# Optimization experiments

Measured on AMD Instinct MI355X. Metric: run time of the kernel, lower is better.

The kernel has to match this reference:

```python
import jax, jax.numpy as jnp
import numpy as np

G, KP, EPS = 4, 9, 1e-5  # deformable groups, 3x3 kernel points, BN eps


def setup_inputs() -> dict:
    key = jax.random.key(0)
    ks = jax.random.split(key, 16)
    N, C1, C2, H, W = 8, 256, 256, 64, 64
    c = int(C1 * 1.0) // 16 * 16  # 256 internal width
    OM = int(np.ceil(G * KP * 3 / 8) * 8)  # 112 padded offset/mask dim (108 used)
    sd = 0.02
    return {
        "x": jax.random.normal(ks[0], (N, C1, H, W), jnp.float32),
        "cv1_w": jax.random.normal(ks[1], (c, C1), jnp.float32) * sd,
        "cv1_b": jax.random.normal(ks[2], (c,), jnp.float32) * sd,
        "value_w": jax.random.normal(ks[3], (c, c), jnp.float32) * sd,
        "value_b": jax.random.normal(ks[4], (c,), jnp.float32) * sd,
        "dw_w": jax.random.normal(ks[5], (c,), jnp.float32) * sd + 1.0,
        "dw_b": jax.random.normal(ks[6], (c,), jnp.float32) * sd,
        "om_w": jax.random.normal(ks[7], (OM, c), jnp.float32) * sd,
        "om_b": jax.random.normal(ks[8], (OM,), jnp.float32) * sd,
        "out_w": jax.random.normal(ks[9], (c, c), jnp.float32) * sd,
        "cv2_w": jax.random.normal(ks[10], (C2, c), jnp.float32) * sd,
        "bn_gamma": jnp.ones((C2,), jnp.float32),
        "bn_beta": jnp.zeros((C2,), jnp.float32),
        "bn_mean": jax.random.normal(ks[11], (C2,), jnp.float32) * 0.1,
        "bn_var": jax.random.uniform(ks[12], (C2,), jnp.float32, minval=0.5, maxval=1.5),
    }


def _dcnv4(value, offset_mask, H, W):
    """DCNv4 core: offset-based bilinear sampling + unnormalized-mask aggregation.
    value: (N,H,W,c) NHWC features; offset_mask: (N,H,W,OM), per group layout
    [2*KP offsets (dx,dy pairs), KP masks]; no softmax on masks (DCNv4)."""
    N, c = value.shape[0], value.shape[-1]
    GC = c // G
    om = offset_mask[..., : G * KP * 3].reshape(N, H, W, G, 3 * KP)
    offs = om[..., : 2 * KP].reshape(N, H, W, G, KP, 2)  # (dx, dy), x = width axis
    mask = om[..., 2 * KP:]                               # (N,H,W,G,KP)
    ky, kx = jnp.meshgrid(jnp.arange(-1, 2, dtype=jnp.float32),
                          jnp.arange(-1, 2, dtype=jnp.float32), indexing="ij")
    kx, ky = kx.reshape(KP), ky.reshape(KP)               # 3x3 dilation-1 grid
    base_x = jnp.arange(W, dtype=jnp.float32)[None, None, :, None, None]
    base_y = jnp.arange(H, dtype=jnp.float32)[None, :, None, None, None]
    px = base_x + kx + offs[..., 0]                       # (N,H,W,G,KP) abs pixel x
    py = base_y + ky + offs[..., 1]
    x0, y0 = jnp.floor(px), jnp.floor(py)
    fx, fy = px - x0, py - y0
    x0i, y0i = x0.astype(jnp.int32), y0.astype(jnp.int32)
    vflat = value.reshape(N, H * W, G, GC).transpose(0, 2, 1, 3)  # (N,G,L,GC)
    acc = jnp.zeros((N, G, H, W, KP, GC), value.dtype)
    for dy, dx, wgt in ((0, 0, (1 - fy) * (1 - fx)), (0, 1, (1 - fy) * fx),
                        (1, 0, fy * (1 - fx)), (1, 1, fy * fx)):
        yy, xx = y0i + dy, x0i + dx
        valid = (yy >= 0) & (yy < H) & (xx >= 0) & (xx < W)   # zero padding
        idx = jnp.clip(yy, 0, H - 1) * W + jnp.clip(xx, 0, W - 1)
        idx_g = idx.transpose(0, 3, 1, 2, 4).reshape(N, G, H * W * KP)
        smp = jnp.take_along_axis(vflat, idx_g[..., None], axis=2)
        smp = smp.reshape(N, G, H, W, KP, GC)
        acc = acc + smp * (wgt * valid).transpose(0, 3, 1, 2, 4)[..., None]
    out = (acc * mask.transpose(0, 3, 1, 2, 4)[..., None]).sum(axis=4)  # (N,G,H,W,GC)
    return out.transpose(0, 2, 3, 1, 4).reshape(N, H, W, c)


def reference(x, cv1_w, cv1_b, value_w, value_b, dw_w, dw_b, om_w, om_b,
              out_w, cv2_w, bn_gamma, bn_beta, bn_mean, bn_var):
    N, C1, H, W = x.shape
    t = jnp.einsum("nchw,dc->nhwd", x, cv1_w) + cv1_b       # cv1 1x1 conv -> NHWC
    value = t @ value_w.T + value_b                          # DCNv4 value_proj
    om = (t * dw_w + dw_b) @ om_w.T + om_b                   # depthwise 1x1 + linear
    y = _dcnv4(value, om, H, W)
    y = y @ out_w.T                                          # output_proj (no bias)
    y = jnp.einsum("nhwc,dc->nhwd", y, cv2_w)                # cv2 1x1 (no bias)
    y = (y - bn_mean) * bn_gamma * jax.lax.rsqrt(bn_var + EPS) + bn_beta  # BN (eval)
    y = y * jax.nn.sigmoid(y)                                # SiLU
    return y.transpose(0, 3, 1, 2)                           # back to NCHW
```

## Files before the change

### kernel.cpp

```cpp
#include <hip/hip_runtime.h>
#include <hip/hip_bf16.h>
#include <math.h>

#define NN    8
#define HH    64
#define WW    64
#define HW    4096
#define NHW   32768
#define DALL  384
#define EPSBN 1e-5f

typedef __attribute__((ext_vector_type(8))) short short8v;
typedef __attribute__((ext_vector_type(4))) float f32x4;
typedef __attribute__((ext_vector_type(2))) float f32x2;

__device__ __forceinline__ float b2f(unsigned short u) {
    union { unsigned int i; float f; } v; v.i = ((unsigned int)u) << 16; return v.f;
}
__device__ __forceinline__ unsigned short f2b(float f) {
    __hip_bfloat16 h = __float2bfloat16(f);
    return *reinterpret_cast<const unsigned short*>(&h);
}
__device__ __forceinline__ f32x2 bf2x(int u) {
    union { int i; float f; } a, b;
    a.i = u << 16;
    b.i = u & 0xffff0000;
    f32x2 r; r[0] = a.f; r[1] = b.f; return r;
}


__global__ __launch_bounds__(256)
void prep_kernel(const float* __restrict__ cv1_w, const float* __restrict__ cv1_b,
                 const float* __restrict__ value_w, const float* __restrict__ value_b,
                 const float* __restrict__ dw_w, const float* __restrict__ dw_b,
                 const float* __restrict__ om_w, const float* __restrict__ om_b,
                 const float* __restrict__ out_w, const float* __restrict__ cv2_w,
                 const float* __restrict__ bn_g, const float* __restrict__ bn_b,
                 const float* __restrict__ bn_m, const float* __restrict__ bn_v,
                 unsigned short* __restrict__ Wallbf, float* __restrict__ ball,
                 unsigned short* __restrict__ Woutbf, float* __restrict__ bout)
{
    int job = blockIdx.x * 256 + threadIdx.x;
    if (job < 65536) {
        int d = job >> 8, cc = job & 255;
        float s0=0.f, s1=0.f, s2=0.f, s3=0.f;
        for (int e = 0; e < 256; e += 4) {
            float4 wv = *reinterpret_cast<const float4*>(&value_w[d*256+e]);
            s0 = fmaf(wv.x, cv1_w[(e+0)*256+cc], s0);
            s1 = fmaf(wv.y, cv1_w[(e+1)*256+cc], s1);
            s2 = fmaf(wv.z, cv1_w[(e+2)*256+cc], s2);
            s3 = fmaf(wv.w, cv1_w[(e+3)*256+cc], s3);
        }
        Wallbf[job] = f2b((s0+s1)+(s2+s3));
    } else if (job < 94208) {
        int idx = job - 65536;
        int o = idx >> 8, cc = idx & 255;
        float s0=0.f, s1=0.f, s2=0.f, s3=0.f;
        for (int e = 0; e < 256; e += 4) {
            float4 wv = *reinterpret_cast<const float4*>(&om_w[o*256+e]);
            float4 dv = *reinterpret_cast<const float4*>(&dw_w[e]);
            s0 = fmaf(wv.x*dv.x, cv1_w[(e+0)*256+cc], s0);
            s1 = fmaf(wv.y*dv.y, cv1_w[(e+1)*256+cc], s1);
            s2 = fmaf(wv.z*dv.z, cv1_w[(e+2)*256+cc], s2);
            s3 = fmaf(wv.w*dv.w, cv1_w[(e+3)*256+cc], s3);
        }
        Wallbf[job] = f2b((s0+s1)+(s2+s3));
    } else if (job < 98304) {
        Wallbf[job] = 0;
    } else if (job < 163840) {
        int idx = job - 98304;
        int d = idx >> 8, cc = idx & 255;
        float s0=0.f, s1=0.f, s2=0.f, s3=0.f;
        for (int e = 0; e < 256; e += 4) {
            float4 wv = *reinterpret_cast<const float4*>(&cv2_w[d*256+e]);
            s0 = fmaf(wv.x, out_w[(e+0)*256+cc], s0);
            s1 = fmaf(wv.y, out_w[(e+1)*256+cc], s1);
            s2 = fmaf(wv.z, out_w[(e+2)*256+cc], s2);
            s3 = fmaf(wv.w, out_w[(e+3)*256+cc], s3);
        }
        float sc = bn_g[d] * rsqrtf(bn_v[d] + EPSBN);
        Woutbf[idx] = f2b(((s0+s1)+(s2+s3)) * sc);
    } else if (job < 164096) {
        int d = job - 163840;
        float s = value_b[d];
        for (int e = 0; e < 256; ++e) s = fmaf(value_w[d*256+e], cv1_b[e], s);
        ball[d] = s;
    } else if (job < 164208) {
        int o = job - 164096;
        float s = om_b[o];
        for (int e = 0; e < 256; ++e)
            s = fmaf(om_w[o*256+e], fmaf(dw_w[e], cv1_b[e], dw_b[e]), s);
        ball[256 + o] = s;
    } else if (job < 164224) {
        ball[368 + job - 164208] = 0.f;
    } else if (job < 164480) {
        int d = job - 164224;
        float sc = bn_g[d] * rsqrtf(bn_v[d] + EPSBN);
        bout[d] = fmaf(-bn_m[d], sc, bn_b[d]);
    }
}

__global__ __launch_bounds__(256)
void gemm_vo_kernel(const float* __restrict__ x, const unsigned short* __restrict__ Wallbf,
                    const float* __restrict__ ball, unsigned short* __restrict__ VO)
{
    __shared__ unsigned short As[8192];
    __shared__ unsigned short Bs[8192];
    int t = threadIdx.x;
    int m0 = blockIdx.y * 128;
    int n0 = blockIdx.x * 128;
    int nimg = m0 >> 12, hw0 = m0 & 4095;
    int lane = t & 63;
    int wv = t >> 6;
    int wr = wv >> 1, wc = wv & 1;
    int r_l = lane & 15, kg_l = lane >> 4;
    int ci = t >> 6;
    int l  = t & 63;

    const float* xbase = x + (size_t)(nimg * 256) * 4096 + hw0;

    f32x4 acc[4][4] = {};

    for (int kt = 0; kt < 4; ++kt) {
        int c0 = kt * 64;
        float2 val[16];
        #pragma unroll
        for (int i = 0; i < 16; ++i)
            val[i] = *reinterpret_cast<const float2*>(
                &xbase[(size_t)(c0 + ci*16 + i) * 4096 + 2*l]);
        __syncthreads();
        #pragma unroll
        for (int rsel = 0; rsel < 2; ++rsel) {
            int row = 2*l + rsel;
            #pragma unroll
            for (int kgi = 0; kgi < 2; ++kgi) {
                int kg = ci*2 + kgi;
                short8v s;
                #pragma unroll
                for (int j = 0; j < 8; ++j)
                    s[j] = (short)f2b(rsel ? val[kgi*8+j].y : val[kgi*8+j].x);
                *reinterpret_cast<short8v*>(&As[row*64 + ((kg ^ (row & 7)) << 3)]) = s;
            }
        }
        #pragma unroll
        for (int i = 0; i < 4; ++i) {
            int idx = t + i*256;
            int row = idx >> 3, kg = idx & 7;
            *reinterpret_cast<short8v*>(&Bs[row*64 + ((kg ^ (row & 7)) << 3)]) =
                *reinterpret_cast<const short8v*>(&Wallbf[(size_t)(n0 + row)*256 + c0 + kg*8]);
        }
        __syncthreads();
        #pragma unroll
        for (int ks = 0; ks < 2; ++ks) {
            short8v af[4], bfr[4];
            #pragma unroll
            for (int m = 0; m < 4; ++m) {
                int row = wr*64 + m*16 + r_l;
                af[m] = *reinterpret_cast<const short8v*>(
                    &As[row*64 + (((ks*4 + kg_l) ^ (row & 7)) << 3)]);
            }
            #pragma unroll
            for (int n = 0; n < 4; ++n) {
                int row = wc*64 + n*16 + r_l;
                bfr[n] = *reinterpret_cast<const short8v*>(
                    &Bs[row*64 + (((ks*4 + kg_l) ^ (row & 7)) << 3)]);
            }
            #pragma unroll
            for (int m = 0; m < 4; ++m)
                #pragma unroll
                for (int n = 0; n < 4; ++n)
                    acc[m][n] = __builtin_amdgcn_mfma_f32_16x16x32_bf16(af[m], bfr[n], acc[m][n], 0, 0, 0);
        }
    }

    #pragma unroll
    for (int n = 0; n < 4; ++n) {
        int d = n0 + wc*64 + n*16 + r_l;
        float bb = ball[d];
        #pragma unroll
        for (int m = 0; m < 4; ++m) {
            int pr = m0 + wr*64 + m*16 + (kg_l << 2);
            #pragma unroll
            for (int r = 0; r < 4; ++r)
                VO[(size_t)(pr + r)*384 + d] = f2b(acc[m][n][r] + bb);
        }
    }
}

__device__ __forceinline__
void gemm_mainloop(const unsigned short* __restrict__ A, const unsigned short* __restrict__ B,
                   int m0, int n0, unsigned short* As, unsigned short* Bs,
                   f32x4 (&acc)[4][4], int t)
{
    int lane = t & 63;
    int wv = t >> 6;
    int wr = wv >> 1, wc = wv & 1;
    int r_l = lane & 15;
    int kg_l = lane >> 4;

    for (int kt = 0; kt < 4; ++kt) {
        int c0 = kt * 64;
        #pragma unroll
        for (int i = 0; i < 4; ++i) {
            int idx = t + i * 256;
            int kg = idx & 7, row = idx >> 3;
            int soff = row*64 + ((kg ^ (row & 7)) << 3);
            *reinterpret_cast<short8v*>(&As[soff]) =
                *reinterpret_cast<const short8v*>(&A[(size_t)(m0 + row)*256 + c0 + kg*8]);
            *reinterpret_cast<short8v*>(&Bs[soff]) =
                *reinterpret_cast<const short8v*>(&B[(size_t)(n0 + row)*256 + c0 + kg*8]);
        }
        __syncthreads();
        #pragma unroll
        for (int ks = 0; ks < 2; ++ks) {
            short8v af[4], bfr[4];
            #pragma unroll
            for (int m = 0; m < 4; ++m) {
                int row = wr*64 + m*16 + r_l;
                af[m] = *reinterpret_cast<const short8v*>(
                    &As[row*64 + (((ks*4 + kg_l) ^ (row & 7)) << 3)]);
            }
            #pragma unroll
            for (int n = 0; n < 4; ++n) {
                int row = wc*64 + n*16 + r_l;
                bfr[n] = *reinterpret_cast<const short8v*>(
                    &Bs[row*64 + (((ks*4 + kg_l) ^ (row & 7)) << 3)]);
            }
            #pragma unroll
            for (int m = 0; m < 4; ++m)
                #pragma unroll
                for (int n = 0; n < 4; ++n)
                    acc[m][n] = __builtin_amdgcn_mfma_f32_16x16x32_bf16(af[m], bfr[n], acc[m][n], 0, 0, 0);
        }
        __syncthreads();
    }
}

__global__ __launch_bounds__(256)
void gemm_out_kernel(const unsigned short* __restrict__ Woutbf, const unsigned short* __restrict__ y,
                     const float* __restrict__ bout, float* __restrict__ out)
{
    __shared__ unsigned short lds[2 * 8192];
    int t = threadIdx.x;
    int m0 = blockIdx.x * 128;
    int n0 = blockIdx.y * 128;
    f32x4 acc[4][4] = {};
    gemm_mainloop(Woutbf, y, m0, n0, lds, lds + 8192, acc, t);

    int lane = t & 63;
    int wv = t >> 6, wr = wv >> 1, wc = wv & 1;
    int r_l = lane & 15, kg_l = lane >> 4;
    int nimg = n0 >> 12;
    int hwb = n0 & 4095;
    #pragma unroll
    for (int m = 0; m < 4; ++m) {
        int dbase = m0 + wr*64 + m*16 + (kg_l << 2);
        #pragma unroll
        for (int r = 0; r < 4; ++r) {
            int d = dbase + r;
            float bb = bout[d];
            #pragma unroll
            for (int n = 0; n < 4; ++n) {
                int pcol = wc*64 + n*16 + r_l;
                float z = acc[m][n][r] + bb;
                float sv = z / (1.f + __expf(-z));
                out[((size_t)(nimg*256 + d))*4096 + hwb + pcol] = sv;
            }
        }
    }
}

__global__ __launch_bounds__(256)
void dcn_kernel(const unsigned short* __restrict__ VO, unsigned short* __restrict__ y)
{
    __shared__ float om_s[8][108];
    int t = threadIdx.x;
    int bid = blockIdx.x;
    int logical = ((bid & 7) << 9) + (bid >> 3);
    int p0 = logical * 8;

    for (int i = t; i < 864; i += 256) {
        int pl = i / 108, j = i - pl * 108;
        om_s[pl][j] = b2f(VO[(size_t)(p0 + pl)*384 + 256 + j]);
    }
    __syncthreads();

    int slot = t >> 3, ch8 = t & 7;
    int pl = slot >> 2, g = slot & 3;
    int p = p0 + pl;
    int hw = p & 4095;
    int h = hw >> 6, w = hw & 63;
    const unsigned short* vbase = VO + (size_t)(p >> 12) * (HW * (size_t)DALL) + g*64 + ch8*8;
    const float* o = &om_s[pl][g*27];

    f32x2 acc2[4] = {};
    #pragma unroll
    for (int k = 0; k < 9; ++k) {
        float dxo = o[2*k], dyo = o[2*k+1], m = o[18+k];
        float pxf = (float)(w + (k % 3) - 1) + dxo;
        float pyf = (float)(h + (k / 3) - 1) + dyo;
        float x0f = floorf(pxf), y0f = floorf(pyf);
        float fx = pxf - x0f, fy = pyf - y0f;
        int x0 = (int)x0f, y0 = (int)y0f;
        #pragma unroll
        for (int dyy = 0; dyy < 2; ++dyy) {
            #pragma unroll
            for (int dxx = 0; dxx < 2; ++dxx) {
                int yy = y0 + dyy, xx = x0 + dxx;
                bool valid = (yy >= 0) & (yy < HH) & (xx >= 0) & (xx < WW);
                float wgt = (dyy ? fy : 1.f - fy) * (dxx ? fx : 1.f - fx);
                float wmc = valid ? (m * wgt) : 0.f;
                int yc = min(max(yy, 0), HH - 1);
                int xc = min(max(xx, 0), WW - 1);
                int4 v = *reinterpret_cast<const int4*>(
                    &vbase[((yc << 6) + xc) * DALL]);
                f32x2 wm2; wm2[0] = wmc; wm2[1] = wmc;
                int vv[4] = {v.x, v.y, v.z, v.w};
                #pragma unroll
                for (int q = 0; q < 4; ++q)
                    acc2[q] += bf2x(vv[q]) * wm2;
            }
        }
    }
    short8v ov;
    #pragma unroll
    for (int q = 0; q < 4; ++q) {
        ov[2*q]   = (short)f2b(acc2[q][0]);
        ov[2*q+1] = (short)f2b(acc2[q][1]);
    }
    *reinterpret_cast<short8v*>(&y[(size_t)p*256 + g*64 + ch8*8]) = ov;
}

extern "C" void kernel_launch(void* const* d_in, const int* in_sizes, int n_in,
                              void* d_out, int out_size, void* d_ws, size_t ws_size,
                              hipStream_t stream) {
    const float* x       = (const float*)d_in[0];
    const float* cv1_w   = (const float*)d_in[1];
    const float* cv1_b   = (const float*)d_in[2];
    const float* value_w = (const float*)d_in[3];
    const float* value_b = (const float*)d_in[4];
    const float* dw_w    = (const float*)d_in[5];
    const float* dw_b    = (const float*)d_in[6];
    const float* om_w    = (const float*)d_in[7];
    const float* om_b    = (const float*)d_in[8];
    const float* out_w   = (const float*)d_in[9];
    const float* cv2_w   = (const float*)d_in[10];
    const float* bn_g    = (const float*)d_in[11];
    const float* bn_b    = (const float*)d_in[12];
    const float* bn_m    = (const float*)d_in[13];
    const float* bn_v    = (const float*)d_in[14];

    char* ws = (char*)d_ws;
    unsigned short* VO     = (unsigned short*)(ws);
    unsigned short* y      = (unsigned short*)(ws + 25165824);
    unsigned short* Wallbf = (unsigned short*)(ws + 41943040);
    unsigned short* Woutbf = (unsigned short*)(ws + 42139648);
    float*          ball   = (float*)(ws + 42270720);
    float*          bout   = (float*)(ws + 42272256);
    float* out = (float*)d_out;

    prep_kernel<<<643, 256, 0, stream>>>(cv1_w, cv1_b, value_w, value_b, dw_w, dw_b,
                                         om_w, om_b, out_w, cv2_w,
                                         bn_g, bn_b, bn_m, bn_v,
                                         Wallbf, ball, Woutbf, bout);
    gemm_vo_kernel<<<dim3(3, 256), 256, 0, stream>>>(x, Wallbf, ball, VO);
    dcn_kernel<<<4096, 256, 0, stream>>>(VO, y);
    gemm_out_kernel<<<dim3(2, 256), 256, 0, stream>>>(Woutbf, y, bout, out);
}
```

Measured before the change: 92.43 us.

## Store value features in zero-padded per-group planes to drop bilinear bounds checks

The value projection output is rewritten from the interleaved 384-wide NHWC buffer into per-image, per-group 68x68 planes with a 2-cell zero border. Offset/mask outputs go to a separate 112-wide buffer. A new kernel zeroes the borders. With the border in place, the deformable sampler clamps sample positions to [-1,64] and reads the four corners directly, with no validity tests or index clamping. The per-group contiguous layout should also make gathers more local. The cost is an extra kernel launch, a slightly larger workspace, and more complex address math in the GEMM epilogue.

```diff
diff --git a/kernel.cpp b/kernel.cpp
--- a/kernel.cpp
+++ b/kernel.cpp
@@ -7,8 +7,11 @@
 #define WW    64
 #define HW    4096
 #define NHW   32768
-#define DALL  384
 #define EPSBN 1e-5f
+
+#define PCELLS   4624
+#define PELEMS   295936
+#define ROWS68   4352
 
 typedef __attribute__((ext_vector_type(8))) short short8v;
 typedef __attribute__((ext_vector_type(4))) float f32x4;
@@ -101,8 +104,37 @@
 }
 
 __global__ __launch_bounds__(256)
+void zero_pad_kernel(unsigned short* __restrict__ V2)
+{
+    int bid = blockIdx.x;
+    unsigned short* base = V2 + (size_t)(bid >> 3) * PELEMS;
+    int off = (bid & 7) * 528;
+    int t = threadIdx.x;
+    for (int ii = t; ii < 528; ii += 256) {
+        int idx = off + ii;
+        int cellsub = idx >> 3;
+        int chunk = idx & 7;
+        int cell;
+        if (cellsub < 272) {
+            int r = cellsub / 68;
+            int c = cellsub - r * 68;
+            int row = (r < 2) ? r : r + 62;
+            cell = row * 68 + c;
+        } else {
+            int i2 = cellsub - 272;
+            int row = 2 + (i2 >> 2);
+            int cs = i2 & 3;
+            int col = (cs < 2) ? cs : cs + 62;
+            cell = row * 68 + col;
+        }
+        *reinterpret_cast<int4*>(&base[cell * 64 + chunk * 8]) = int4{0,0,0,0};
+    }
+}
+
+__global__ __launch_bounds__(256)
 void gemm_vo_kernel(const float* __restrict__ x, const unsigned short* __restrict__ Wallbf,
-                    const float* __restrict__ ball, unsigned short* __restrict__ VO)
+                    const float* __restrict__ ball,
+                    unsigned short* __restrict__ V2, unsigned short* __restrict__ OM)
 {
     __shared__ unsigned short As[8192];
     __shared__ unsigned short Bs[8192];
@@ -181,8 +213,19 @@
         for (int m = 0; m < 4; ++m) {
             int pr = m0 + wr*64 + m*16 + (kg_l << 2);
             #pragma unroll
-            for (int r = 0; r < 4; ++r)
-                VO[(size_t)(pr + r)*384 + d] = f2b(acc[m][n][r] + bb);
+            for (int r = 0; r < 4; ++r) {
+                float res = acc[m][n][r] + bb;
+                int p = pr + r;
+                if (d < 256) {
+                    int g = d >> 6, ch = d & 63;
+                    int hw = p & 4095;
+                    int yy = hw >> 6, xx = hw & 63;
+                    size_t cell = (size_t)((p >> 12)*4 + g) * PCELLS + (yy + 2)*68 + (xx + 2);
+                    V2[cell * 64 + ch] = f2b(res);
+                } else if (d < 368) {
+                    OM[(size_t)p * 112 + (d - 256)] = f2b(res);
+                }
+            }
         }
     }
 }
@@ -271,7 +314,8 @@
 }
 
 __global__ __launch_bounds__(256)
-void dcn_kernel(const unsigned short* __restrict__ VO, unsigned short* __restrict__ y)
+void dcn_kernel(const unsigned short* __restrict__ V2, const unsigned short* __restrict__ OM,
+                unsigned short* __restrict__ y)
 {
     __shared__ float om_s[8][108];
     int t = threadIdx.x;
@@ -281,7 +325,7 @@
 
     for (int i = t; i < 864; i += 256) {
         int pl = i / 108, j = i - pl * 108;
-        om_s[pl][j] = b2f(VO[(size_t)(p0 + pl)*384 + 256 + j]);
+        om_s[pl][j] = b2f(OM[(size_t)(p0 + pl)*112 + j]);
     }
     __syncthreads();
 
@@ -290,38 +334,54 @@
     int p = p0 + pl;
     int hw = p & 4095;
     int h = hw >> 6, w = hw & 63;
-    const unsigned short* vbase = VO + (size_t)(p >> 12) * (HW * (size_t)DALL) + g*64 + ch8*8;
+    const unsigned short* plane =
+        V2 + (size_t)((p >> 12)*4 + g) * PELEMS + ch8*8;
     const float* o = &om_s[pl][g*27];
 
     f32x2 acc2[4] = {};
     #pragma unroll
     for (int k = 0; k < 9; ++k) {
         float dxo = o[2*k], dyo = o[2*k+1], m = o[18+k];
-        float pxf = (float)(w + (k % 3) - 1) + dxo;
-        float pyf = (float)(h + (k / 3) - 1) + dyo;
-        float x0f = floorf(pxf), y0f = floorf(pyf);
-        float fx = pxf - x0f, fy = pyf - y0f;
-        int x0 = (int)x0f, y0 = (int)y0f;
-        #pragma unroll
-        for (int dyy = 0; dyy < 2; ++dyy) {
-            #pragma unroll
-            for (int dxx = 0; dxx < 2; ++dxx) {
-                int yy = y0 + dyy, xx = x0 + dxx;
-                bool valid = (yy >= 0) & (yy < HH) & (xx >= 0) & (xx < WW);
-                float wgt = (dyy ? fy : 1.f - fy) * (dxx ? fx : 1.f - fx);
-                float wmc = valid ? (m * wgt) : 0.f;
-                int yc = min(max(yy, 0), HH - 1);
-                int xc = min(max(xx, 0), WW - 1);
-                int4 v = *reinterpret_cast<const int4*>(
-                    &vbase[((yc << 6) + xc) * DALL]);
-                f32x2 wm2; wm2[0] = wmc; wm2[1] = wmc;
-                int vv[4] = {v.x, v.y, v.z, v.w};
-                #pragma unroll
-                for (int q = 0; q < 4; ++q)
-                    acc2[q] += bf2x(vv[q]) * wm2;
-            }
-        }
-    }
+        float px = fminf(fmaxf((float)(w + (k % 3) - 1) + dxo, -1.f), 64.f);
+        float py = fminf(fmaxf((float)(h + (k / 3) - 1) + dyo, -1.f), 64.f);
+        float x0f = floorf(px), y0f = floorf(py);
+        float fx = px - x0f, fy = py - y0f;
+        float gx = 1.f - fx, gy = 1.f - fy;
+        int cell = ((int)y0f + 2) * 68 + ((int)x0f + 2);
+        const unsigned short* cp0 = plane + cell * 64;
+        const unsigned short* cp1 = cp0 + ROWS68;
+        int4 v00 = *reinterpret_cast<const int4*>(cp0);
+        int4 v01 = *reinterpret_cast<const int4*>(cp0 + 64);
+        int4 v10 = *reinterpret_cast<const int4*>(cp1);
+        int4 v11 = *reinterpret_cast<const int4*>(cp1 + 64);
+        float gym = gy * m, fym = fy * m;
+        float w00 = gym*gx, w01 = gym*fx, w10 = fym*gx, w11 = fym*fx;
+        {
+            f32x2 W; W[0] = w00; W[1] = w00;
+            int a[4] = {v00.x, v00.y, v00.z, v00.w};
+            #pragma unroll
+            for (int q = 0; q < 4; ++q) acc2[q] += bf2x(a[q]) * W;
+        }
+        {
+            f32x2 W; W[0] = w01; W[1] = w01;
+            int a[4] = {v01.x, v01.y, v01.z, v01.w};
+            #pragma unroll
+            for (int q = 0; q < 4; ++q) acc2[q] += bf2x(a[q]) * W;
+        }
+        {
+            f32x2 W; W[0] = w10; W[1] = w10;
+            int a[4] = {v10.x, v10.y, v10.z, v10.w};
+            #pragma unroll
+            for (int q = 0; q < 4; ++q) acc2[q] += bf2x(a[q]) * W;
+        }
+        {
+            f32x2 W; W[0] = w11; W[1] = w11;
+            int a[4] = {v11.x, v11.y, v11.z, v11.w};
+            #pragma unroll
+            for (int q = 0; q < 4; ++q) acc2[q] += bf2x(a[q]) * W;
+        }
+    }
+
     short8v ov;
     #pragma unroll
     for (int q = 0; q < 4; ++q) {
@@ -351,19 +411,21 @@
     const float* bn_v    = (const float*)d_in[14];
 
     char* ws = (char*)d_ws;
-    unsigned short* VO     = (unsigned short*)(ws);
-    unsigned short* y      = (unsigned short*)(ws + 25165824);
-    unsigned short* Wallbf = (unsigned short*)(ws + 41943040);
-    unsigned short* Woutbf = (unsigned short*)(ws + 42139648);
-    float*          ball   = (float*)(ws + 42270720);
-    float*          bout   = (float*)(ws + 42272256);
+    unsigned short* V2     = (unsigned short*)(ws);
+    unsigned short* OM     = (unsigned short*)(ws + 18939904);
+    unsigned short* y      = (unsigned short*)(ws + 26279936);
+    unsigned short* Wallbf = (unsigned short*)(ws + 43057152);
+    unsigned short* Woutbf = (unsigned short*)(ws + 43253760);
+    float*          ball   = (float*)(ws + 43384832);
+    float*          bout   = (float*)(ws + 43386368);
     float* out = (float*)d_out;
 
     prep_kernel<<<643, 256, 0, stream>>>(cv1_w, cv1_b, value_w, value_b, dw_w, dw_b,
                                          om_w, om_b, out_w, cv2_w,
                                          bn_g, bn_b, bn_m, bn_v,
                                          Wallbf, ball, Woutbf, bout);
-    gemm_vo_kernel<<<dim3(3, 256), 256, 0, stream>>>(x, Wallbf, ball, VO);
-    dcn_kernel<<<4096, 256, 0, stream>>>(VO, y);
+    zero_pad_kernel<<<256, 256, 0, stream>>>(V2);
+    gemm_vo_kernel<<<dim3(3, 256), 256, 0, stream>>>(x, Wallbf, ball, V2, OM);
+    dcn_kernel<<<4096, 256, 0, stream>>>(V2, OM, y);
     gemm_out_kernel<<<dim3(2, 256), 256, 0, stream>>>(Woutbf, y, bout, out);
 }
```

After: 93.52 us. Within noise of the previous version (+1.2%).

## Fuse deformable sampling with output GEMM via LDS-resident y tile

Applied to the files above, without the earlier changes.

Merges the DCN sampling kernel and the output-projection GEMM into one kernel. Each 512-thread block samples one image row of 64 pixels into a swizzled LDS y tile, then multiplies it against all 256 output channels of the weight matrix, staged in LDS, and applies bias and SiLU. This removes the global round-trip of the 16MB bf16 y buffer and one kernel launch. In exchange the grid shrinks to 512 blocks, weights are reloaded by every block, and the GEMM tile becomes narrower (256x64), which may lower MFMA efficiency and occupancy because of the 64KB of LDS per block.

```diff
diff --git a/kernel.cpp b/kernel.cpp
--- a/kernel.cpp
+++ b/kernel.cpp
@@ -187,33 +187,100 @@
     }
 }
 
-__device__ __forceinline__
-void gemm_mainloop(const unsigned short* __restrict__ A, const unsigned short* __restrict__ B,
-                   int m0, int n0, unsigned short* As, unsigned short* Bs,
-                   f32x4 (&acc)[4][4], int t)
+__global__ __launch_bounds__(512, 4)
+void dcn_gemm_kernel(const unsigned short* __restrict__ VO,
+                     const unsigned short* __restrict__ Woutbf,
+                     const float* __restrict__ bout, float* __restrict__ out)
 {
+    __shared__ unsigned short y_lds[16384];
+    __shared__ char u_buf[32768];
+    float* om_s = reinterpret_cast<float*>(u_buf);
+    unsigned short* As = reinterpret_cast<unsigned short*>(u_buf);
+
+    int t = threadIdx.x;
+    int bid = blockIdx.x;
+    int logical = ((bid & 7) << 6) + (bid >> 3);
+    int p0 = logical * 64;
+    int nimg = p0 >> 12;
+    int hw0 = p0 & 4095;
+    int h = hw0 >> 6;
+
+    const unsigned short* vimg = VO + (size_t)nimg * (HW * (size_t)DALL);
+
+    for (int i = t; i < 6912; i += 512) {
+        int pl = i / 108, j = i - pl * 108;
+        om_s[pl * 108 + j] = b2f(vimg[(size_t)(hw0 + pl) * DALL + 256 + j]);
+    }
+    __syncthreads();
+
+    int ch8 = t & 7;
+    #pragma unroll
+    for (int iter = 0; iter < 4; ++iter) {
+        int slotIdx = iter * 64 + (t >> 3);
+        int px = slotIdx >> 2, g = slotIdx & 3;
+        int w = px;
+        const unsigned short* vbase = vimg + g*64 + ch8*8;
+        const float* o = om_s + px*108 + g*27;
+
+        f32x2 acc2[4] = {};
+        #pragma unroll
+        for (int k = 0; k < 9; ++k) {
+            float dxo = o[2*k], dyo = o[2*k+1], m = o[18+k];
+            float pxf = (float)(w + (k % 3) - 1) + dxo;
+            float pyf = (float)(h + (k / 3) - 1) + dyo;
+            float x0f = floorf(pxf), y0f = floorf(pyf);
+            float fx = pxf - x0f, fy = pyf - y0f;
+            int x0 = (int)x0f, y0 = (int)y0f;
+            #pragma unroll
+            for (int dyy = 0; dyy < 2; ++dyy) {
+                #pragma unroll
+                for (int dxx = 0; dxx < 2; ++dxx) {
+                    int yy = y0 + dyy, xx = x0 + dxx;
+                    bool valid = (yy >= 0) & (yy < HH) & (xx >= 0) & (xx < WW);
+                    float wgt = (dyy ? fy : 1.f - fy) * (dxx ? fx : 1.f - fx);
+                    float wmc = valid ? (m * wgt) : 0.f;
+                    int yc = min(max(yy, 0), HH - 1);
+                    int xc = min(max(xx, 0), WW - 1);
+                    int4 v = *reinterpret_cast<const int4*>(
+                        &vbase[((yc << 6) + xc) * DALL]);
+                    f32x2 wm2; wm2[0] = wmc; wm2[1] = wmc;
+                    int vv[4] = {v.x, v.y, v.z, v.w};
+                    #pragma unroll
+                    for (int q = 0; q < 4; ++q)
+                        acc2[q] += bf2x(vv[q]) * wm2;
+                }
+            }
+        }
+        short8v ov;
+        #pragma unroll
+        for (int q = 0; q < 4; ++q) {
+            ov[2*q]   = (short)f2b(acc2[q][0]);
+            ov[2*q+1] = (short)f2b(acc2[q][1]);
+        }
+        *reinterpret_cast<short8v*>(
+            &y_lds[g*4096 + px*64 + ((ch8 ^ (px & 7)) << 3)]) = ov;
+    }
+
     int lane = t & 63;
     int wv = t >> 6;
     int wr = wv >> 1, wc = wv & 1;
-    int r_l = lane & 15;
-    int kg_l = lane >> 4;
-
+    int r_l = lane & 15, kg_l = lane >> 4;
+
+    f32x4 acc[4][2] = {};
     for (int kt = 0; kt < 4; ++kt) {
         int c0 = kt * 64;
+        __syncthreads();
         #pragma unroll
         for (int i = 0; i < 4; ++i) {
-            int idx = t + i * 256;
-            int kg = idx & 7, row = idx >> 3;
-            int soff = row*64 + ((kg ^ (row & 7)) << 3);
-            *reinterpret_cast<short8v*>(&As[soff]) =
-                *reinterpret_cast<const short8v*>(&A[(size_t)(m0 + row)*256 + c0 + kg*8]);
-            *reinterpret_cast<short8v*>(&Bs[soff]) =
-                *reinterpret_cast<const short8v*>(&B[(size_t)(n0 + row)*256 + c0 + kg*8]);
+            int idx = t + i * 512;
+            int row = idx >> 3, kg = idx & 7;
+            *reinterpret_cast<short8v*>(&As[row*64 + ((kg ^ (row & 7)) << 3)]) =
+                *reinterpret_cast<const short8v*>(&Woutbf[(size_t)row*256 + c0 + kg*8]);
         }
         __syncthreads();
         #pragma unroll
         for (int ks = 0; ks < 2; ++ks) {
-            short8v af[4], bfr[4];
+            short8v af[4], bfr[2];
             #pragma unroll
             for (int m = 0; m < 4; ++m) {
                 int row = wr*64 + m*16 + r_l;
@@ -221,114 +288,35 @@
                     &As[row*64 + (((ks*4 + kg_l) ^ (row & 7)) << 3)]);
             }
             #pragma unroll
-            for (int n = 0; n < 4; ++n) {
-                int row = wc*64 + n*16 + r_l;
+            for (int n = 0; n < 2; ++n) {
+                int row = wc*32 + n*16 + r_l;
                 bfr[n] = *reinterpret_cast<const short8v*>(
-                    &Bs[row*64 + (((ks*4 + kg_l) ^ (row & 7)) << 3)]);
+                    &y_lds[kt*4096 + row*64 + (((ks*4 + kg_l) ^ (row & 7)) << 3)]);
             }
             #pragma unroll
             for (int m = 0; m < 4; ++m)
                 #pragma unroll
-                for (int n = 0; n < 4; ++n)
+                for (int n = 0; n < 2; ++n)
                     acc[m][n] = __builtin_amdgcn_mfma_f32_16x16x32_bf16(af[m], bfr[n], acc[m][n], 0, 0, 0);
         }
-        __syncthreads();
-    }
-}
-
-__global__ __launch_bounds__(256)
-void gemm_out_kernel(const unsigned short* __restrict__ Woutbf, const unsigned short* __restrict__ y,
-                     const float* __restrict__ bout, float* __restrict__ out)
-{
-    __shared__ unsigned short lds[2 * 8192];
-    int t = threadIdx.x;
-    int m0 = blockIdx.x * 128;
-    int n0 = blockIdx.y * 128;
-    f32x4 acc[4][4] = {};
-    gemm_mainloop(Woutbf, y, m0, n0, lds, lds + 8192, acc, t);
-
-    int lane = t & 63;
-    int wv = t >> 6, wr = wv >> 1, wc = wv & 1;
-    int r_l = lane & 15, kg_l = lane >> 4;
-    int nimg = n0 >> 12;
-    int hwb = n0 & 4095;
+    }
+
     #pragma unroll
     for (int m = 0; m < 4; ++m) {
-        int dbase = m0 + wr*64 + m*16 + (kg_l << 2);
+        int dbase = wr*64 + m*16 + (kg_l << 2);
         #pragma unroll
         for (int r = 0; r < 4; ++r) {
             int d = dbase + r;
             float bb = bout[d];
             #pragma unroll
-            for (int n = 0; n < 4; ++n) {
-                int pcol = wc*64 + n*16 + r_l;
+            for (int n = 0; n < 2; ++n) {
+                int pcol = wc*32 + n*16 + r_l;
                 float z = acc[m][n][r] + bb;
                 float sv = z / (1.f + __expf(-z));
-                out[((size_t)(nimg*256 + d))*4096 + hwb + pcol] = sv;
-            }
-        }
-    }
-}
-
-__global__ __launch_bounds__(256)
-void dcn_kernel(const unsigned short* __restrict__ VO, unsigned short* __restrict__ y)
-{
-    __shared__ float om_s[8][108];
-    int t = threadIdx.x;
-    int bid = blockIdx.x;
-    int logical = ((bid & 7) << 9) + (bid >> 3);
-    int p0 = logical * 8;
-
-    for (int i = t; i < 864; i += 256) {
-        int pl = i / 108, j = i - pl * 108;
-        om_s[pl][j] = b2f(VO[(size_t)(p0 + pl)*384 + 256 + j]);
-    }
-    __syncthreads();
-
-    int slot = t >> 3, ch8 = t & 7;
-    int pl = slot >> 2, g = slot & 3;
-    int p = p0 + pl;
-    int hw = p & 4095;
-    int h = hw >> 6, w = hw & 63;
-    const unsigned short* vbase = VO + (size_t)(p >> 12) * (HW * (size_t)DALL) + g*64 + ch8*8;
-    const float* o = &om_s[pl][g*27];
-
-    f32x2 acc2[4] = {};
-    #pragma unroll
-    for (int k = 0; k < 9; ++k) {
-        float dxo = o[2*k], dyo = o[2*k+1], m = o[18+k];
-        float pxf = (float)(w + (k % 3) - 1) + dxo;
-        float pyf = (float)(h + (k / 3) - 1) + dyo;
-        float x0f = floorf(pxf), y0f = floorf(pyf);
-        float fx = pxf - x0f, fy = pyf - y0f;
-        int x0 = (int)x0f, y0 = (int)y0f;
-        #pragma unroll
-        for (int dyy = 0; dyy < 2; ++dyy) {
-            #pragma unroll
-            for (int dxx = 0; dxx < 2; ++dxx) {
-                int yy = y0 + dyy, xx = x0 + dxx;
-                bool valid = (yy >= 0) & (yy < HH) & (xx >= 0) & (xx < WW);
-                float wgt = (dyy ? fy : 1.f - fy) * (dxx ? fx : 1.f - fx);
-                float wmc = valid ? (m * wgt) : 0.f;
-                int yc = min(max(yy, 0), HH - 1);
-                int xc = min(max(xx, 0), WW - 1);
-                int4 v = *reinterpret_cast<const int4*>(
-                    &vbase[((yc << 6) + xc) * DALL]);
-                f32x2 wm2; wm2[0] = wmc; wm2[1] = wmc;
-                int vv[4] = {v.x, v.y, v.z, v.w};
-                #pragma unroll
-                for (int q = 0; q < 4; ++q)
-                    acc2[q] += bf2x(vv[q]) * wm2;
-            }
-        }
-    }
-    short8v ov;
-    #pragma unroll
-    for (int q = 0; q < 4; ++q) {
-        ov[2*q]   = (short)f2b(acc2[q][0]);
-        ov[2*q+1] = (short)f2b(acc2[q][1]);
-    }
-    *reinterpret_cast<short8v*>(&y[(size_t)p*256 + g*64 + ch8*8]) = ov;
+                out[((size_t)(nimg*256 + d))*4096 + hw0 + pcol] = sv;
+            }
+        }
+    }
 }
 
 extern "C" void kernel_launch(void* const* d_in, const int* in_sizes, int n_in,
@@ -352,11 +340,10 @@
 
     char* ws = (char*)d_ws;
     unsigned short* VO     = (unsigned short*)(ws);
-    unsigned short* y      = (unsigned short*)(ws + 25165824);
-    unsigned short* Wallbf = (unsigned short*)(ws + 41943040);
-    unsigned short* Woutbf = (unsigned short*)(ws + 42139648);
-    float*          ball   = (float*)(ws + 42270720);
-    float*          bout   = (float*)(ws + 42272256);
+    unsigned short* Wallbf = (unsigned short*)(ws + 25165824);
+    unsigned short* Woutbf = (unsigned short*)(ws + 25362432);
+    float*          ball   = (float*)(ws + 25493504);
+    float*          bout   = (float*)(ws + 25495040);
     float* out = (float*)d_out;
 
     prep_kernel<<<643, 256, 0, stream>>>(cv1_w, cv1_b, value_w, value_b, dw_w, dw_b,
@@ -364,6 +351,5 @@
                                          bn_g, bn_b, bn_m, bn_v,
                                          Wallbf, ball, Woutbf, bout);
     gemm_vo_kernel<<<dim3(3, 256), 256, 0, stream>>>(x, Wallbf, ball, VO);
-    dcn_kernel<<<4096, 256, 0, stream>>>(VO, y);
-    gemm_out_kernel<<<dim3(2, 256), 256, 0, stream>>>(Woutbf, y, bout, out);
-}
+    dcn_gemm_kernel<<<512, 512, 0, stream>>>(VO, Woutbf, bout, out);
+}
```

Measured after the change: 88.96 us, median of 2. 1.04x faster.
